# Kernel optimization log

Hardware: AMD Instinct MI355X
Metric: run time of the kernel (lower is better)

## Reference

```python
import jax, jax.numpy as jnp
import numpy as np

D = 256      # d_model
H = 8        # nhead
HD = D // H  # head_dim
B = 16       # ragged batch size
L = 4096     # tokens per sample (equal lengths here; code handles general ragged)
NQ = 100     # instance queries per sample


def _xavier(key, shape):
    a = float(np.sqrt(6.0 / (shape[0] + shape[1])))
    return jax.random.uniform(key, shape, jnp.float32, -a, a)


def setup_inputs() -> dict:
    key = jax.random.key(0)
    ks = jax.random.split(key, 8)
    total = B * L
    source = jax.random.normal(ks[0], (total, D), jnp.float32)
    query = jax.random.normal(ks[1], (B, NQ, D), jnp.float32)
    batch_offsets = (jnp.arange(B + 1) * L).astype(jnp.int32)
    # nn.MultiheadAttention params: in-proj (split into q/k/v) + out-proj.
    Wq = _xavier(ks[2], (D, D)); bq = jnp.zeros((D,), jnp.float32)
    Wk = _xavier(ks[3], (D, D)); bk = jnp.zeros((D,), jnp.float32)
    Wv = _xavier(ks[4], (D, D)); bv = jnp.zeros((D,), jnp.float32)
    Wo = _xavier(ks[5], (D, D)); bo = jnp.zeros((D,), jnp.float32)
    return {"source": source, "query": query, "batch_offsets": batch_offsets,
            "Wq": Wq, "bq": bq, "Wk": Wk, "bk": bk, "Wv": Wv, "bv": bv,
            "Wo": Wo, "bo": bo}


def reference(source, query, batch_offsets, Wq, bq, Wk, bk, Wv, bv, Wo, bo):
    # Ragged -> padded gather (indices are concrete, computed with numpy).
    offs = np.asarray(batch_offsets)
    lens = offs[1:] - offs[:-1]                      # (B,)
    Lmax = int(lens.max())
    pos = np.arange(Lmax)
    mask = pos[None, :] < lens[:, None]              # (B, Lmax) valid keys
    idx = np.where(mask, offs[:-1, None] + pos[None, :], 0)
    kv_in = source[jnp.asarray(idx)]                 # (B, Lmax, D)

    # Projections (torch Linear: x @ W.T + b), split into heads.
    q = (query @ Wq.T + bq).reshape(B, NQ, H, HD)
    k = (kv_in @ Wk.T + bk).reshape(B, Lmax, H, HD)
    v = (kv_in @ Wv.T + bv).reshape(B, Lmax, H, HD)

    scale = 1.0 / jnp.sqrt(jnp.asarray(HD, q.dtype))
    scores = jnp.einsum("bqhd,bkhd->bhqk", q * scale, k)
    scores = jnp.where(jnp.asarray(mask)[:, None, None, :], scores, -1e30)
    attn = jax.nn.softmax(scores, axis=-1)           # (B, H, NQ, Lmax)
    ctx = jnp.einsum("bhqk,bkhd->bqhd", attn, v).reshape(B, NQ, D)
    out = ctx @ Wo.T + bo
    # Original code: dropout/norm results are discarded; residual add of query.
    return out + query
```

## Files before the change

### kernel.cpp

```cpp
#include <hip/hip_runtime.h>
#include <hip/hip_bf16.h>
#include <math.h>

#define DM     256
#define NHEAD  8
#define HDIM   32
#define QPAD   112
#define NCHUNK 8
#define BM     64
#define BN     256
#define BK     32
#define ALD    264
#define CQ     4
#define MAXB   64

typedef __attribute__((ext_vector_type(8))) short bf16x8;
typedef __attribute__((ext_vector_type(4))) short bf16x4;
typedef __attribute__((ext_vector_type(4))) float f32x4;

__device__ __forceinline__ short f2bf(float f) {
  union { float f; unsigned u; } x; x.f = f;
  unsigned u = (x.u + 0x7fffu + ((x.u >> 16) & 1u)) >> 16;
  return (short)u;
}
__device__ __forceinline__ float bf2f(short s) {
  union { unsigned u; float f; } x; x.u = ((unsigned)(unsigned short)s) << 16;
  return x.f;
}
__device__ __forceinline__ bf16x8 bzero8() {
  bf16x8 v;
#pragma unroll
  for (int j = 0; j < 8; j++) v[j] = (short)0;
  return v;
}
__device__ __forceinline__ bf16x8 cvt8(const float* p) {
  float4 x0 = *(const float4*)p, x1 = *(const float4*)(p + 4);
  bf16x8 v;
  v[0] = f2bf(x0.x); v[1] = f2bf(x0.y); v[2] = f2bf(x0.z); v[3] = f2bf(x0.w);
  v[4] = f2bf(x1.x); v[5] = f2bf(x1.y); v[6] = f2bf(x1.z); v[7] = f2bf(x1.w);
  return v;
}
__device__ __forceinline__ bf16x8 cvt8s(const float* p, float s) {
  float4 x0 = *(const float4*)p, x1 = *(const float4*)(p + 4);
  bf16x8 v;
  v[0] = f2bf(x0.x * s); v[1] = f2bf(x0.y * s);
  v[2] = f2bf(x0.z * s); v[3] = f2bf(x0.w * s);
  v[4] = f2bf(x1.x * s); v[5] = f2bf(x1.y * s);
  v[6] = f2bf(x1.z * s); v[7] = f2bf(x1.w * s);
  return v;
}

__global__ __launch_bounds__(256) void wconv_kernel(
    const float* __restrict__ Wk, const float* __restrict__ Wv,
    const float* __restrict__ Wq, short* __restrict__ Wkvq) {
  int idx = blockIdx.x * 256 + threadIdx.x;
  int e0 = idx * 8;
  const float* p;
  float s = 1.f;
  if (e0 < DM * DM) {
    p = Wk + e0;
  } else if (e0 < 2 * DM * DM) {
    p = Wv + (e0 - DM * DM);
  } else {
    p = Wq + (e0 - 2 * DM * DM);
    s = 0.17677669529663687f;
  }
  *(bf16x8*)(Wkvq + e0) = cvt8s(p, s);
}

__global__ __launch_bounds__(256) void kv_gemm_kernel(
    const float* __restrict__ src, const float* __restrict__ query,
    const short* __restrict__ Wkvq, const float* __restrict__ bq,
    const float* __restrict__ bk, const float* __restrict__ bv,
    const int* __restrict__ offs, short* __restrict__ Qw,
    short* __restrict__ Kw, short* __restrict__ Vw, int T, int Bn, int NQ,
    int Mtiles, int kvb) {
  int bid = blockIdx.x;
  int tid = threadIdx.x;
  int wave = tid >> 6, lane = tid & 63;
  int l15 = lane & 15, quad = lane >> 4;

  bool isQ = (bid >= kvb);
  const float* Asrc;
  int Arows, t0, n0;
  bool swapped;
  bool isK = false;
  if (isQ) {
    int qt = bid - kvb;
    t0 = qt * BM;
    Asrc = query;
    Arows = Bn * NQ;
    n0 = 2 * DM;
    swapped = true;
  } else {
    int mtile = (bid >> 4) * 8 + (bid & 7);
    int ntile = (bid >> 3) & 1;
    if (mtile >= Mtiles) return;
    t0 = mtile * BM;
    n0 = ntile * BN;
    isK = (ntile == 0);
    swapped = isK;
    Asrc = src;
    Arows = T;
  }

  __shared__ __align__(16) short As[BM * ALD];
  __shared__ int obuf[MAXB + 1];

  f32x4 acc[4][4];
#pragma unroll
  for (int i = 0; i < 4; i++)
#pragma unroll
    for (int j = 0; j < 4; j++) acc[i][j] = (f32x4){0.f, 0.f, 0.f, 0.f};

  {
    int arow = tid >> 2, ac4 = tid & 3;
    int atok = t0 + arow;
    if (atok >= Arows) atok = Arows - 1;
    const float* arp = Asrc + (size_t)atok * DM;
#pragma unroll
    for (int r = 0; r < 4; r++) {
      int c0 = r * 64 + ac4 * 16;
      const float* p = arp + c0;
      bf16x8 v0 = cvt8(p);
      bf16x8 v1 = cvt8(p + 8);
      *(bf16x8*)&As[arow * ALD + c0]     = v0;
      *(bf16x8*)&As[arow * ALD + c0 + 8] = v1;
    }
    if (tid <= Bn && tid <= MAXB) obuf[tid] = offs[tid];
  }
  __syncthreads();

  const short* bptr = Wkvq + (size_t)(n0 + wave * 64 + l15) * DM + quad * 8;
#pragma unroll
  for (int kk = 0; kk < DM; kk += BK) {
    bf16x8 bf_[4];
#pragma unroll
    for (int nt = 0; nt < 4; nt++)
      bf_[nt] = *(const bf16x8*)(bptr + (size_t)nt * 16 * DM + kk);
    bf16x8 af[4];
#pragma unroll
    for (int mt = 0; mt < 4; mt++)
      af[mt] = *(const bf16x8*)&As[(mt * 16 + l15) * ALD + kk + quad * 8];
    if (swapped) {
#pragma unroll
      for (int mt = 0; mt < 4; mt++)
#pragma unroll
        for (int nt = 0; nt < 4; nt++)
          acc[mt][nt] = __builtin_amdgcn_mfma_f32_16x16x32_bf16(
              bf_[nt], af[mt], acc[mt][nt], 0, 0, 0);
    } else {
#pragma unroll
      for (int mt = 0; mt < 4; mt++)
#pragma unroll
        for (int nt = 0; nt < 4; nt++)
          acc[mt][nt] = __builtin_amdgcn_mfma_f32_16x16x32_bf16(
              af[mt], bf_[nt], acc[mt][nt], 0, 0, 0);
    }
  }

  if (isQ) {
    const float scale = 0.17677669529663687f;
    float bq4[4][4];
    int hQ[4], hdQ[4];
#pragma unroll
    for (int nt = 0; nt < 4; nt++) {
      int nbq = wave * 64 + nt * 16 + quad * 4;
      float4 b4 = *(const float4*)(bq + nbq);
      bq4[nt][0] = b4.x * scale; bq4[nt][1] = b4.y * scale;
      bq4[nt][2] = b4.z * scale; bq4[nt][3] = b4.w * scale;
      hQ[nt] = nbq >> 5;
      hdQ[nt] = nbq & 31;
    }
#pragma unroll
    for (int mt = 0; mt < 4; mt++) {
      int row = t0 + mt * 16 + l15;
      if (row >= Arows) continue;
      int b = row / NQ;
      int q = row - b * NQ;
#pragma unroll
      for (int nt = 0; nt < 4; nt++) {
        bf16x4 p;
#pragma unroll
        for (int r = 0; r < 4; r++) p[r] = f2bf(acc[mt][nt][r] + bq4[nt][r]);
        *(bf16x4*)&Qw[(((size_t)b * NHEAD + hQ[nt]) * QPAD + q) * HDIM +
                      hdQ[nt]] = p;
      }
    }
  } else if (isK) {
    const float* bias = bk;
    float bk4[4][4];
    int hK[4], hdK[4];
#pragma unroll
    for (int nt = 0; nt < 4; nt++) {
      int nbq = wave * 64 + nt * 16 + quad * 4;
      float4 b4 = *(const float4*)(bias + nbq);
      bk4[nt][0] = b4.x; bk4[nt][1] = b4.y; bk4[nt][2] = b4.z; bk4[nt][3] = b4.w;
      hK[nt] = nbq >> 5;
      hdK[nt] = nbq & 31;
    }
    int bcur = 0;
#pragma unroll
    for (int mt = 0; mt < 4; mt++) {
      int tok = t0 + mt * 16 + l15;
      if (tok >= T) continue;
      while (bcur + 1 < Bn && obuf[bcur + 1] <= tok) bcur++;
      int off = obuf[bcur], len = obuf[bcur + 1] - off;
      int l = tok - off;
      size_t bb = (size_t)off * DM;
#pragma unroll
      for (int nt = 0; nt < 4; nt++) {
        bf16x4 p;
#pragma unroll
        for (int r = 0; r < 4; r++) p[r] = f2bf(acc[mt][nt][r] + bk4[nt][r]);
        *(bf16x4*)&Kw[bb + (size_t)hK[nt] * len * HDIM + (size_t)l * HDIM +
                      hdK[nt]] = p;
      }
    }
  } else {
    const float* bias = bv;
    float bV[4];
    int hV[4], hdV[4];
#pragma unroll
    for (int nt = 0; nt < 4; nt++) {
      int nb = wave * 64 + nt * 16 + l15;
      bV[nt] = bias[nb];
      hV[nt] = nb >> 5;
      hdV[nt] = nb & 31;
    }
    int bcur = 0;
#pragma unroll
    for (int mt = 0; mt < 4; mt++) {
      int tb = t0 + mt * 16 + quad * 4;
      if (tb >= T) continue;
      while (bcur + 1 < Bn && obuf[bcur + 1] <= tb) bcur++;
      int off = obuf[bcur], len = obuf[bcur + 1] - off;
      size_t bb = (size_t)off * DM;
      bool span = (tb + 3 < obuf[bcur + 1]) && (tb + 3 < T);
      if (span) {
        int l = tb - off;
#pragma unroll
        for (int nt = 0; nt < 4; nt++) {
          size_t idx =
              bb + (size_t)hV[nt] * len * HDIM + (size_t)hdV[nt] * len + l;
          bf16x4 p;
#pragma unroll
          for (int r = 0; r < 4; r++) p[r] = f2bf(acc[mt][nt][r] + bV[nt]);
          if ((idx & 3) == 0) {
            *(bf16x4*)&Vw[idx] = p;
          } else {
#pragma unroll
            for (int r = 0; r < 4; r++) Vw[idx + r] = p[r];
          }
        }
      } else {
        int bc2 = bcur;
#pragma unroll
        for (int r = 0; r < 4; r++) {
          int tok = tb + r;
          if (tok >= T) continue;
          while (bc2 + 1 < Bn && obuf[bc2 + 1] <= tok) bc2++;
          int off2 = obuf[bc2], len2 = obuf[bc2 + 1] - off2;
          int l = tok - off2;
          size_t bb2 = (size_t)off2 * DM;
#pragma unroll
          for (int nt = 0; nt < 4; nt++)
            Vw[bb2 + (size_t)hV[nt] * len2 * HDIM + (size_t)hdV[nt] * len2 +
               l] = f2bf(acc[mt][nt][r] + bV[nt]);
        }
      }
    }
  }
}

__global__ __launch_bounds__(448) void attn_kernel(
    const short* __restrict__ Qw, const short* __restrict__ Kw,
    const short* __restrict__ Vw, const int* __restrict__ offs,
    short* __restrict__ Ops, float* __restrict__ Ml, int Bn) {
  int c  = blockIdx.x % NCHUNK;
  int bh = blockIdx.x / NCHUNK;
  int h = bh % NHEAD, b = bh / NHEAD;
  int wave = threadIdx.x >> 6, lane = threadIdx.x & 63;
  int l15 = lane & 15, quad = lane >> 4;

  int off = offs[b], len = offs[b + 1] - off;
  int cl = ((len + NCHUNK * 32 - 1) / (NCHUNK * 32)) * 32;
  int kstart = c * cl;
  int kend   = min(kstart + cl, len);

  const short* Kh = Kw + (size_t)off * DM + (size_t)h * len * HDIM;
  const short* Vh = Vw + (size_t)off * DM + (size_t)h * len * HDIM;

  int row16 = wave * 16 + l15;
  bf16x8 aq = *(const bf16x8*)(
      Qw + (((size_t)b * NHEAD + h) * QPAD + row16) * HDIM + quad * 8);

  f32x4 o[2];
#pragma unroll
  for (int j = 0; j < 2; j++) o[j] = (f32x4){0.f, 0.f, 0.f, 0.f};
  float mrun[4], lrun[4];
#pragma unroll
  for (int r = 0; r < 4; r++) { mrun[r] = -1e30f; lrun[r] = 0.f; }

  __shared__ __align__(16) short plds[7][16][72];

  for (int kb = kstart; kb < kend; kb += 64) {
    bool valid[4];
    bf16x8 bk_[4];
#pragma unroll
    for (int nt = 0; nt < 4; nt++) {
      int key = kb + nt * 16 + l15;
      valid[nt] = key < kend;
      bk_[nt] = valid[nt]
                    ? *(const bf16x8*)(Kh + (size_t)key * HDIM + quad * 8)
                    : bzero8();
    }
    f32x4 zero = {0.f, 0.f, 0.f, 0.f};
    f32x4 s[4];
#pragma unroll
    for (int nt = 0; nt < 4; nt++)
      s[nt] = __builtin_amdgcn_mfma_f32_16x16x32_bf16(aq, bk_[nt], zero, 0, 0, 0);
#pragma unroll
    for (int r = 0; r < 4; r++) {
      float v0 = valid[0] ? s[0][r] : -1e30f;
      float v1 = valid[1] ? s[1][r] : -1e30f;
      float v2 = valid[2] ? s[2][r] : -1e30f;
      float v3 = valid[3] ? s[3][r] : -1e30f;
      float t = fmaxf(fmaxf(v0, v1), fmaxf(v2, v3));
      t = fmaxf(t, __shfl_xor(t, 1, 16));
      t = fmaxf(t, __shfl_xor(t, 2, 16));
      t = fmaxf(t, __shfl_xor(t, 4, 16));
      t = fmaxf(t, __shfl_xor(t, 8, 16));
      float mn = fmaxf(mrun[r], t);
      float al = __expf(mrun[r] - mn);
      float p0 = valid[0] ? __expf(v0 - mn) : 0.f;
      float p1 = valid[1] ? __expf(v1 - mn) : 0.f;
      float p2 = valid[2] ? __expf(v2 - mn) : 0.f;
      float p3 = valid[3] ? __expf(v3 - mn) : 0.f;
      lrun[r] = al * lrun[r] + ((p0 + p1) + (p2 + p3));
      mrun[r] = mn;
      o[0][r] *= al;
      o[1][r] *= al;
      plds[wave][quad * 4 + r][l15]      = f2bf(p0);
      plds[wave][quad * 4 + r][16 + l15] = f2bf(p1);
      plds[wave][quad * 4 + r][32 + l15] = f2bf(p2);
      plds[wave][quad * 4 + r][48 + l15] = f2bf(p3);
    }
    bf16x8 pa0 = *(const bf16x8*)&plds[wave][l15][quad * 8];
    bf16x8 pa1 = *(const bf16x8*)&plds[wave][l15][32 + quad * 8];
    bf16x8 bv_[2][2];
#pragma unroll
    for (int half = 0; half < 2; half++) {
#pragma unroll
      for (int ht = 0; ht < 2; ht++) {
        int hd = ht * 16 + l15;
        int k0 = kb + half * 32 + quad * 8;
        const short* p = Vh + (size_t)hd * len + k0;
        if (k0 + 7 < len) {
          bv_[half][ht] = *(const bf16x8*)p;
        } else {
          bf16x8 v;
#pragma unroll
          for (int j = 0; j < 8; j++) v[j] = (k0 + j < len) ? p[j] : (short)0;
          bv_[half][ht] = v;
        }
      }
    }
#pragma unroll
    for (int ht = 0; ht < 2; ht++) {
      o[ht] = __builtin_amdgcn_mfma_f32_16x16x32_bf16(pa0, bv_[0][ht], o[ht],
                                                      0, 0, 0);
      o[ht] = __builtin_amdgcn_mfma_f32_16x16x32_bf16(pa1, bv_[1][ht], o[ht],
                                                      0, 0, 0);
    }
  }

#pragma unroll
  for (int r = 0; r < 4; r++) {
    lrun[r] += __shfl_xor(lrun[r], 1, 16);
    lrun[r] += __shfl_xor(lrun[r], 2, 16);
    lrun[r] += __shfl_xor(lrun[r], 4, 16);
    lrun[r] += __shfl_xor(lrun[r], 8, 16);
  }

#pragma unroll
  for (int r = 0; r < 4; r++) {
    int row = wave * 16 + quad * 4 + r;
    size_t base = (((size_t)c * Bn + b) * NHEAD + h) * QPAD + row;
#pragma unroll
    for (int ht = 0; ht < 2; ht++)
      Ops[base * HDIM + ht * 16 + l15] = f2bf(o[ht][r]);
    if (l15 == 0) {
      Ml[base * 2]     = mrun[r];
      Ml[base * 2 + 1] = lrun[r];
    }
  }
}

__global__ __launch_bounds__(256) void combine_kernel(
    const short* __restrict__ Ops, const float* __restrict__ Ml,
    const float* __restrict__ query, const float* __restrict__ Wo,
    const float* __restrict__ bo, float* __restrict__ out, int Bn, int NQ) {
  int bpb = (NQ + CQ - 1) / CQ;
  int b  = blockIdx.x / bpb;
  int q0 = (blockIdx.x % bpb) * CQ;
  int tid = threadIdx.x;

  __shared__ __align__(16) short opsl[CQ][NCHUNK][DM];
  __shared__ float mll[NCHUNK][NHEAD][CQ][2];
  __shared__ __align__(16) float ctx[CQ * DM];

  for (int t = tid; t < CQ * NCHUNK * (DM / 8); t += 256) {
    int q   = t / (NCHUNK * 32);
    int rem = t % (NCHUNK * 32);
    int c   = rem / 32;
    int v   = rem % 32;
    int h   = v >> 2;
    int hd0 = (v & 3) * 8;
    int qq = q0 + q;
    if (qq >= NQ) qq = NQ - 1;
    size_t base = (((size_t)c * Bn + b) * NHEAD + h) * QPAD + qq;
    *(bf16x8*)&opsl[q][c][v * 8] = *(const bf16x8*)&Ops[base * HDIM + hd0];
  }
  for (int t = tid; t < CQ * NCHUNK * NHEAD; t += 256) {
    int q   = t / (NCHUNK * NHEAD);
    int rem = t % (NCHUNK * NHEAD);
    int c   = rem / NHEAD;
    int h   = rem % NHEAD;
    int qq = q0 + q;
    if (qq >= NQ) qq = NQ - 1;
    size_t base = (((size_t)c * Bn + b) * NHEAD + h) * QPAD + qq;
    mll[c][h][q][0] = Ml[base * 2];
    mll[c][h][q][1] = Ml[base * 2 + 1];
  }
  __syncthreads();

  int d = tid, h = d >> 5;
#pragma unroll
  for (int qi = 0; qi < CQ; qi++) {
    float M = -1e30f;
#pragma unroll
    for (int c = 0; c < NCHUNK; c++) M = fmaxf(M, mll[c][h][qi][0]);
    float L = 0.f, acc = 0.f;
#pragma unroll
    for (int c = 0; c < NCHUNK; c++) {
      float w = __expf(mll[c][h][qi][0] - M);
      L += mll[c][h][qi][1] * w;
      acc += w * bf2f(opsl[qi][c][d]);
    }
    ctx[qi * DM + d] = (L > 0.f) ? acc / L : 0.f;
  }
  __syncthreads();

  const float* wrow = Wo + (size_t)d * DM;
  float acc[CQ];
  float bias = bo[d];
#pragma unroll
  for (int qi = 0; qi < CQ; qi++) acc[qi] = bias;
  for (int k = 0; k < DM; k += 4) {
    float4 w = *(const float4*)(wrow + k);
#pragma unroll
    for (int qi = 0; qi < CQ; qi++) {
      float4 x = *(const float4*)&ctx[qi * DM + k];
      acc[qi] += x.x * w.x + x.y * w.y + x.z * w.z + x.w * w.w;
    }
  }
#pragma unroll
  for (int qi = 0; qi < CQ; qi++) {
    int q = q0 + qi;
    if (q < NQ)
      out[((size_t)b * NQ + q) * DM + d] =
          acc[qi] + query[((size_t)b * NQ + q) * DM + d];
  }
}

extern "C" void kernel_launch(void* const* d_in, const int* in_sizes, int n_in,
                              void* d_out, int out_size, void* d_ws,
                              size_t ws_size, hipStream_t stream) {
  const float* src   = (const float*)d_in[0];
  const float* query = (const float*)d_in[1];
  const int*   offs  = (const int*)d_in[2];
  const float* Wq = (const float*)d_in[3];
  const float* bq = (const float*)d_in[4];
  const float* Wk = (const float*)d_in[5];
  const float* bk = (const float*)d_in[6];
  const float* Wv = (const float*)d_in[7];
  const float* bv = (const float*)d_in[8];
  const float* Wo = (const float*)d_in[9];
  const float* bo = (const float*)d_in[10];
  float* out = (float*)d_out;

  int T  = in_sizes[0] / DM;
  int Bn = in_sizes[2] - 1;
  int NQ = in_sizes[1] / (Bn * DM);

  char* w = (char*)d_ws;
  size_t qsz = (size_t)Bn * NHEAD * QPAD * HDIM * 2;
  size_t ksz = (size_t)T * DM * 2;
  size_t osz = (size_t)NCHUNK * Bn * NHEAD * QPAD * HDIM * 2;
  size_t msz = (size_t)NCHUNK * Bn * NHEAD * QPAD * 2 * 4;
  short* Qw  = (short*)w;
  short* Kw  = (short*)(w + qsz);
  short* Vw  = (short*)(w + qsz + ksz);
  short* Ops = (short*)(w + qsz + 2 * ksz);
  float* Mlp = (float*)(w + qsz + 2 * ksz + osz);
  short* Wkvq = (short*)(w + qsz + 2 * ksz + osz + msz);

  int Mtiles = (T + BM - 1) / BM;
  int groups = (Mtiles + 7) / 8;
  int kvb = groups * 16;
  int qtiles = (Bn * NQ + BM - 1) / BM;

  wconv_kernel<<<(3 * DM * DM) / (256 * 8), 256, 0, stream>>>(Wk, Wv, Wq,
                                                              Wkvq);
  kv_gemm_kernel<<<kvb + qtiles, 256, 0, stream>>>(
      src, query, Wkvq, bq, bk, bv, offs, Qw, Kw, Vw, T, Bn, NQ, Mtiles, kvb);
  attn_kernel<<<Bn * NHEAD * NCHUNK, 448, 0, stream>>>(Qw, Kw, Vw, offs, Ops,
                                                       Mlp, Bn);
  combine_kernel<<<Bn * ((NQ + CQ - 1) / CQ), 256, 0, stream>>>(
      Ops, Mlp, query, Wo, bo, out, Bn, NQ);
}
```

Baseline: 228.8 us.

## Compute both K and V projections per source tile in one block

Each KV-projection block now loads its 64-token source tile into shared memory once and runs two GEMM passes, first K and then V, instead of launching separate blocks for the K and V column halves. This halves the global reads and fp32-to-bf16 conversion of the source activations and halves the number of blocks in that phase. In exchange each block does twice the serial MFMA work, the grid shrinks, and there is less parallelism to hide latency.

Result: faster. 222.4 us, median of 2 (-2.8%).

```diff
diff --git a/kernel.cpp b/kernel.cpp
--- a/kernel.cpp
+++ b/kernel.cpp
@@ -68,6 +68,45 @@
   *(bf16x8*)(Wkvq + e0) = cvt8s(p, s);
 }
 
+#define ZERO_ACC()                                          \
+  _Pragma("unroll")                                         \
+  for (int zi = 0; zi < 4; zi++)                            \
+    _Pragma("unroll")                                       \
+    for (int zj = 0; zj < 4; zj++)                          \
+      acc[zi][zj] = (f32x4){0.f, 0.f, 0.f, 0.f};
+
+#define KLOOP(N0, SWAP)                                                      \
+  {                                                                          \
+    const short* bptr =                                                      \
+        Wkvq + (size_t)((N0) + wave * 64 + l15) * DM + quad * 8;             \
+    _Pragma("unroll")                                                        \
+    for (int kk = 0; kk < DM; kk += BK) {                                    \
+      bf16x8 bf_[4];                                                         \
+      _Pragma("unroll")                                                      \
+      for (int nt = 0; nt < 4; nt++)                                         \
+        bf_[nt] = *(const bf16x8*)(bptr + (size_t)nt * 16 * DM + kk);        \
+      bf16x8 af[4];                                                          \
+      _Pragma("unroll")                                                      \
+      for (int mt = 0; mt < 4; mt++)                                         \
+        af[mt] = *(const bf16x8*)&As[(mt * 16 + l15) * ALD + kk + quad * 8]; \
+      if (SWAP) {                                                            \
+        _Pragma("unroll")                                                    \
+        for (int mt = 0; mt < 4; mt++)                                       \
+          _Pragma("unroll")                                                  \
+          for (int nt = 0; nt < 4; nt++)                                     \
+            acc[mt][nt] = __builtin_amdgcn_mfma_f32_16x16x32_bf16(           \
+                bf_[nt], af[mt], acc[mt][nt], 0, 0, 0);                      \
+      } else {                                                               \
+        _Pragma("unroll")                                                    \
+        for (int mt = 0; mt < 4; mt++)                                       \
+          _Pragma("unroll")                                                  \
+          for (int nt = 0; nt < 4; nt++)                                     \
+            acc[mt][nt] = __builtin_amdgcn_mfma_f32_16x16x32_bf16(           \
+                af[mt], bf_[nt], acc[mt][nt], 0, 0, 0);                      \
+      }                                                                      \
+    }                                                                        \
+  }
+
 __global__ __launch_bounds__(256) void kv_gemm_kernel(
     const float* __restrict__ src, const float* __restrict__ query,
     const short* __restrict__ Wkvq, const float* __restrict__ bq,
@@ -82,24 +121,13 @@
 
   bool isQ = (bid >= kvb);
   const float* Asrc;
-  int Arows, t0, n0;
-  bool swapped;
-  bool isK = false;
+  int Arows, t0;
   if (isQ) {
-    int qt = bid - kvb;
-    t0 = qt * BM;
+    t0 = (bid - kvb) * BM;
     Asrc = query;
     Arows = Bn * NQ;
-    n0 = 2 * DM;
-    swapped = true;
   } else {
-    int mtile = (bid >> 4) * 8 + (bid & 7);
-    int ntile = (bid >> 3) & 1;
-    if (mtile >= Mtiles) return;
-    t0 = mtile * BM;
-    n0 = ntile * BN;
-    isK = (ntile == 0);
-    swapped = isK;
+    t0 = bid * BM;
     Asrc = src;
     Arows = T;
   }
@@ -108,10 +136,6 @@
   __shared__ int obuf[MAXB + 1];
 
   f32x4 acc[4][4];
-#pragma unroll
-  for (int i = 0; i < 4; i++)
-#pragma unroll
-    for (int j = 0; j < 4; j++) acc[i][j] = (f32x4){0.f, 0.f, 0.f, 0.f};
 
   {
     int arow = tid >> 2, ac4 = tid & 3;
@@ -131,35 +155,9 @@
   }
   __syncthreads();
 
-  const short* bptr = Wkvq + (size_t)(n0 + wave * 64 + l15) * DM + quad * 8;
-#pragma unroll
-  for (int kk = 0; kk < DM; kk += BK) {
-    bf16x8 bf_[4];
-#pragma unroll
-    for (int nt = 0; nt < 4; nt++)
-      bf_[nt] = *(const bf16x8*)(bptr + (size_t)nt * 16 * DM + kk);
-    bf16x8 af[4];
-#pragma unroll
-    for (int mt = 0; mt < 4; mt++)
-      af[mt] = *(const bf16x8*)&As[(mt * 16 + l15) * ALD + kk + quad * 8];
-    if (swapped) {
-#pragma unroll
-      for (int mt = 0; mt < 4; mt++)
-#pragma unroll
-        for (int nt = 0; nt < 4; nt++)
-          acc[mt][nt] = __builtin_amdgcn_mfma_f32_16x16x32_bf16(
-              bf_[nt], af[mt], acc[mt][nt], 0, 0, 0);
-    } else {
-#pragma unroll
-      for (int mt = 0; mt < 4; mt++)
-#pragma unroll
-        for (int nt = 0; nt < 4; nt++)
-          acc[mt][nt] = __builtin_amdgcn_mfma_f32_16x16x32_bf16(
-              af[mt], bf_[nt], acc[mt][nt], 0, 0, 0);
-    }
-  }
-
   if (isQ) {
+    ZERO_ACC();
+    KLOOP(2 * DM, 1);
     const float scale = 0.17677669529663687f;
     float bq4[4][4];
     int hQ[4], hdQ[4];
@@ -187,7 +185,12 @@
                       hdQ[nt]] = p;
       }
     }
-  } else if (isK) {
+    return;
+  }
+
+  ZERO_ACC();
+  KLOOP(0, 1);
+  {
     const float* bias = bk;
     float bk4[4][4];
     int hK[4], hdK[4];
@@ -217,7 +220,11 @@
                       hdK[nt]] = p;
       }
     }
-  } else {
+  }
+
+  ZERO_ACC();
+  KLOOP(DM, 0);
+  {
     const float* bias = bv;
     float bV[4];
     int hV[4], hdV[4];
@@ -507,14 +514,13 @@
   short* Wkvq = (short*)(w + qsz + 2 * ksz + osz + msz);
 
   int Mtiles = (T + BM - 1) / BM;
-  int groups = (Mtiles + 7) / 8;
-  int kvb = groups * 16;
   int qtiles = (Bn * NQ + BM - 1) / BM;
 
   wconv_kernel<<<(3 * DM * DM) / (256 * 8), 256, 0, stream>>>(Wk, Wv, Wq,
                                                               Wkvq);
-  kv_gemm_kernel<<<kvb + qtiles, 256, 0, stream>>>(
-      src, query, Wkvq, bq, bk, bv, offs, Qw, Kw, Vw, T, Bn, NQ, Mtiles, kvb);
+  kv_gemm_kernel<<<Mtiles + qtiles, 256, 0, stream>>>(
+      src, query, Wkvq, bq, bk, bv, offs, Qw, Kw, Vw, T, Bn, NQ, Mtiles,
+      Mtiles);
   attn_kernel<<<Bn * NHEAD * NCHUNK, 448, 0, stream>>>(Qw, Kw, Vw, offs, Ops,
                                                        Mlp, Bn);
   combine_kernel<<<Bn * ((NQ + CQ - 1) / CQ), 256, 0, stream>>>(
```
